# Kernel optimization log

Hardware: AMD Instinct MI355X
Metric: run time of the kernel (lower is better)

The kernel has to match this reference:

```python
import jax, jax.numpy as jnp
import numpy as np

B, S, D, H = 2, 2048, 1024, 16
HD = D // H  # 64


def setup_inputs() -> dict:
    key = jax.random.key(0)
    ks = jax.random.split(key, 7)
    s = 1.0 / np.sqrt(HD)
    return {
        "x": jax.random.normal(ks[0], (B, S, D), dtype=jnp.float32),
        "Wq": jax.random.normal(ks[1], (H, HD, HD), dtype=jnp.float32) * s,
        "bq": jax.random.normal(ks[2], (H, HD), dtype=jnp.float32) * 0.01,
        "Wk": jax.random.normal(ks[3], (H, HD, HD), dtype=jnp.float32) * s,
        "bk": jax.random.normal(ks[4], (H, HD), dtype=jnp.float32) * 0.01,
        "Wv": jax.random.normal(ks[5], (H, HD, HD), dtype=jnp.float32) * s,
        "bv": jax.random.normal(ks[6], (H, HD), dtype=jnp.float32) * 0.01,
    }


def reference(x, Wq, bq, Wk, bk, Wv, bv):
    b, s, d = x.shape
    h, hd, _ = Wq.shape
    # Faithful to torch: x.view(B, H, S, hd) is a raw reshape (mixes seq positions
    # across heads), NOT a transpose-based head split.
    xh = x.reshape(b, h, s, hd)
    # torch Linear: y @ W.T + b, with W of shape (out, in)
    q = jnp.einsum('bhse,hde->bhsd', xh, Wq) + bq[None, :, None, :]
    k = jnp.einsum('bhse,hde->bhsd', xh, Wk) + bk[None, :, None, :]
    v = jnp.einsum('bhse,hde->bhsd', xh, Wv) + bv[None, :, None, :]
    scale = 1.0 / jnp.sqrt(jnp.asarray(d / h, dtype=jnp.float32))
    attn = jax.nn.softmax(jnp.einsum('bhqd,bhkd->bhqk', q, k) * scale, axis=-1)
    out = jnp.einsum('bhqk,bhkd->bhqd', attn, v)
    # torch.cat over heads along last dim == transpose then merge
    return out.transpose(0, 2, 1, 3).reshape(b, s, d)
```

## Files before the change

### kernel.cpp

```cpp
#include <hip/hip_runtime.h>
#include <hip/hip_bf16.h>

#define BATCH 2
#define SEQ   2048
#define DMODEL 1024
#define NH    16
#define HD    64
#define QSCALE 0.1803368801111602f

typedef __attribute__((ext_vector_type(8))) short bf16x8;
typedef __attribute__((ext_vector_type(4))) float f32x4;

__device__ __forceinline__ ushort f2bf(float f) {
    union { float f; unsigned u; } v; v.f = f;
    return (ushort)((v.u + 0x8000u) >> 16);
}

__device__ __forceinline__ unsigned pack2bf(float a, float b) {
    union { float f; unsigned u; } x, y; x.f = a; y.f = b;
    return __builtin_amdgcn_perm(y.u + 0x8000u, x.u + 0x8000u, 0x07060302u);
}

__device__ __forceinline__ float exp2r(float x) {
#if __has_builtin(__builtin_amdgcn_exp2f)
    return __builtin_amdgcn_exp2f(x);
#else
    return exp2f(x);
#endif
}

#define MFMA(a, b, c) __builtin_amdgcn_mfma_f32_16x16x32_bf16((a), (b), (c), 0, 0, 0)

__global__ __launch_bounds__(256) void wfmt_kernel(
    const float* __restrict__ Wq, const float* __restrict__ Wk,
    const float* __restrict__ Wv, ushort* __restrict__ Wf)
{
    const int blk = blockIdx.x;
    const int h = blk / 3, m = blk - h * 3;
    const float* W = (m == 0 ? Wq : (m == 1 ? Wk : Wv)) + h * 4096;
    const float s = (m == 0) ? QSCALE : 1.0f;
    for (int i = 0; i < 2; ++i) {
        int idx = threadIdx.x + 256 * i;
        int l = idx & 63, chunk = idx >> 6;
        int qd = l >> 4, l16 = l & 15, nt = chunk >> 1, ks = chunk & 1;
        const float* src = W + (nt * 16 + l16) * 64 + ks * 32 + qd * 8;
        float4 a = *(const float4*)src;
        float4 b = *(const float4*)(src + 4);
        union { bf16x8 v; unsigned u[4]; } t;
        t.u[0] = pack2bf(a.x * s, a.y * s);
        t.u[1] = pack2bf(a.z * s, a.w * s);
        t.u[2] = pack2bf(b.x * s, b.y * s);
        t.u[3] = pack2bf(b.z * s, b.w * s);
        *(bf16x8*)&Wf[((size_t)blk * 512 + idx) * 8] = t.v;
    }
}

__global__ __launch_bounds__(256) void qkv_kernel(
    const float* __restrict__ x, const ushort* __restrict__ Wf,
    const float* __restrict__ bq, const float* __restrict__ bk,
    const float* __restrict__ bv,
    ushort* __restrict__ Qo, ushort* __restrict__ Kf, ushort* __restrict__ Vf)
{
    const int bid = blockIdx.x;
    const int st  = bid & 31;
    const int bh  = bid >> 5;
    const int h   = bh & (NH - 1);

    __shared__ ushort EbQ[64 * 72];
    __shared__ ushort EbK[64 * 72];
    __shared__ ushort EbV[64 * 72];

    const int tid  = threadIdx.x;
    const int wave = tid >> 6, lane = tid & 63;
    const int ln16 = lane & 15, quad = lane >> 4;

    const float* xr = x + (size_t)bh * (SEQ * HD)
                        + ((size_t)st * 64 + wave * 16 + ln16) * HD;
    bf16x8 afr[2];
#pragma unroll
    for (int ks = 0; ks < 2; ++ks) {
        const float4* p = (const float4*)(xr + ks * 32 + quad * 8);
        float4 a = p[0], b = p[1];
        union { bf16x8 v; unsigned u[4]; } t;
        t.u[0] = pack2bf(a.x, a.y);
        t.u[1] = pack2bf(a.z, a.w);
        t.u[2] = pack2bf(b.x, b.y);
        t.u[3] = pack2bf(b.z, b.w);
        afr[ks] = t.v;
    }

    const bf16x8* wf = (const bf16x8*)Wf + (size_t)h * 1536 + lane;

    f32x4 acc[3][4];
#pragma unroll
    for (int m = 0; m < 3; ++m)
#pragma unroll
        for (int nt = 0; nt < 4; ++nt) {
            f32x4 a = {0.f, 0.f, 0.f, 0.f};
            a = MFMA(afr[0], wf[(m * 8 + nt * 2 + 0) * 64], a);
            a = MFMA(afr[1], wf[(m * 8 + nt * 2 + 1) * 64], a);
            acc[m][nt] = a;
        }

#pragma unroll
    for (int nt = 0; nt < 4; ++nt) {
        float bbq = bq[h * 64 + nt * 16 + ln16] * QSCALE;
        float bbk = bk[h * 64 + nt * 16 + ln16];
#pragma unroll
        for (int r = 0; r < 4; ++r) {
            EbQ[(wave * 16 + quad * 4 + r) * 72 + nt * 16 + ln16] = f2bf(acc[0][nt][r] + bbq);
            EbK[(wave * 16 + quad * 4 + r) * 72 + nt * 16 + ln16] = f2bf(acc[1][nt][r] + bbk);
        }
        float bbv = bv[h * 64 + nt * 16 + ln16];
        ushort4 o;
        o.x = f2bf(acc[2][nt][0] + bbv);
        o.y = f2bf(acc[2][nt][1] + bbv);
        o.z = f2bf(acc[2][nt][2] + bbv);
        o.w = f2bf(acc[2][nt][3] + bbv);
        *(ushort4*)&EbV[(nt * 16 + ln16) * 72 + wave * 16 + quad * 4] = o;
    }
    __syncthreads();

    {
        ushort* dst = Qo + (size_t)bh * SEQ * HD + (size_t)st * 64 * HD;
        for (int i = 0; i < 2; ++i) {
            int idx = tid + 256 * i;
            int row = idx >> 3, c8 = (idx & 7) * 8;
            *(bf16x8*)&dst[row * 64 + c8] = *(const bf16x8*)&EbQ[row * 72 + c8];
        }
    }
    {
        ushort* dstK = Kf + ((size_t)bh * 32 + st) * 4096;
        ushort* dstV = Vf + ((size_t)bh * 32 + st) * 4096;
        for (int i = 0; i < 2; ++i) {
            int idx8 = tid + 256 * i;
            int l2 = idx8 & 63, chunk = idx8 >> 6;
            int nt = chunk >> 1, ks = chunk & 1;
            int qd = l2 >> 4, l16 = l2 & 15;
            *(bf16x8*)&dstK[(size_t)idx8 * 8] =
                *(const bf16x8*)&EbK[(nt * 16 + l16) * 72 + ks * 32 + qd * 8];
            *(bf16x8*)&dstV[(size_t)idx8 * 8] =
                *(const bf16x8*)&EbV[(nt * 16 + l16) * 72 + ks * 32 + qd * 8];
        }
    }
}

__global__ __launch_bounds__(512, 4) void attn_kernel(
    const ushort* __restrict__ Q, const ushort* __restrict__ Kf,
    const ushort* __restrict__ Vf, float* __restrict__ out)
{
    const int bid = blockIdx.x;
    const int wid = (bid & 7) * 64 + (bid >> 3);
    const int qt  = wid & 15;
    const int bh  = wid >> 4;
    const int h   = bh & (NH - 1), b = bh >> 4;

    __shared__ ushort Ps[8][2][2048];

    const int tid = threadIdx.x, wave = tid >> 6, lane = tid & 63;
    const int ln16 = lane & 15, quad = lane >> 4;
    const int qw = wave & 3, kh = wave >> 2;
    const unsigned swz = (unsigned)(ln16 & 7) << 4;

    bf16x8 qfr[2][2];
#pragma unroll
    for (int g = 0; g < 2; ++g) {
        const ushort* Qg = Q + ((size_t)bh * SEQ + qt * 128 + qw * 32 + g * 16 + ln16) * HD;
        qfr[g][0] = *(const bf16x8*)&Qg[quad * 8];
        qfr[g][1] = *(const bf16x8*)&Qg[32 + quad * 8];
    }

    const bf16x8* kfp = (const bf16x8*)(Kf + (size_t)bh * 32 * 4096) + kh * 8192 + lane;
    const bf16x8* vfp = (const bf16x8*)(Vf + (size_t)bh * 32 * 4096) + kh * 8192 + lane;

    float lsum[2] = {0.f, 0.f};
    f32x4 accO[2][4];
#pragma unroll
    for (int g = 0; g < 2; ++g)
#pragma unroll
        for (int nt = 0; nt < 4; ++nt) accO[g][nt] = (f32x4){0.f, 0.f, 0.f, 0.f};

    bf16x8 kf[8], vf[8];
#pragma unroll
    for (int c = 0; c < 8; ++c) kf[c] = kfp[c * 64];
    kfp += 512;

    for (int kt = 0; kt < 16; ++kt) {
        const int cur = kt & 1;

        f32x4 sacc[2][4];
#pragma unroll
        for (int nt = 0; nt < 4; ++nt)
#pragma unroll
            for (int g = 0; g < 2; ++g) {
                f32x4 a = {0.f, 0.f, 0.f, 0.f};
                a = MFMA(kf[nt * 2],     qfr[g][0], a);
                a = MFMA(kf[nt * 2 + 1], qfr[g][1], a);
                sacc[g][nt] = a;
            }

        if (kt < 15) {
#pragma unroll
            for (int c = 0; c < 8; ++c) kf[c] = kfp[c * 64];
            kfp += 512;
        }

        if (kt > 0) {
            const char* Pr = (const char*)Ps[wave][1 - cur];
            bf16x8 pf[2][2];
#pragma unroll
            for (int g = 0; g < 2; ++g) {
                const char* Prr = Pr + (g * 16 + ln16) * 128;
                pf[g][0] = *(const bf16x8*)(Prr + (((unsigned)(quad * 16)) ^ swz));
                pf[g][1] = *(const bf16x8*)(Prr + (((unsigned)(64 + quad * 16)) ^ swz));
            }
#pragma unroll
            for (int nt = 0; nt < 4; ++nt)
#pragma unroll
                for (int g = 0; g < 2; ++g) {
                    accO[g][nt] = MFMA(vf[nt * 2],     pf[g][0], accO[g][nt]);
                    accO[g][nt] = MFMA(vf[nt * 2 + 1], pf[g][1], accO[g][nt]);
                }
        }

#pragma unroll
        for (int c = 0; c < 8; ++c) vf[c] = vfp[c * 64];
        vfp += 512;

        char* Pw = (char*)Ps[wave][cur];
#pragma unroll
        for (int g = 0; g < 2; ++g) {
            char* Pwr = Pw + (g * 16 + ln16) * 128;
            float rs = 0.f;
#pragma unroll
            for (int nt = 0; nt < 4; ++nt) {
                float p0 = exp2r(sacc[g][nt][0]);
                float p1 = exp2r(sacc[g][nt][1]);
                float p2 = exp2r(sacc[g][nt][2]);
                float p3 = exp2r(sacc[g][nt][3]);
                rs += (p0 + p1) + (p2 + p3);
                uint2 pk;
                pk.x = pack2bf(p0, p1);
                pk.y = pack2bf(p2, p3);
                *(uint2*)(Pwr + (((unsigned)(nt * 32 + quad * 8)) ^ swz)) = pk;
            }
            lsum[g] += rs;
        }
    }

    {
        const char* Pr = (const char*)Ps[wave][1];
        bf16x8 pf[2][2];
#pragma unroll
        for (int g = 0; g < 2; ++g) {
            const char* Prr = Pr + (g * 16 + ln16) * 128;
            pf[g][0] = *(const bf16x8*)(Prr + (((unsigned)(quad * 16)) ^ swz));
            pf[g][1] = *(const bf16x8*)(Prr + (((unsigned)(64 + quad * 16)) ^ swz));
        }
#pragma unroll
        for (int nt = 0; nt < 4; ++nt)
#pragma unroll
            for (int g = 0; g < 2; ++g) {
                accO[g][nt] = MFMA(vf[nt * 2],     pf[g][0], accO[g][nt]);
                accO[g][nt] = MFMA(vf[nt * 2 + 1], pf[g][1], accO[g][nt]);
            }
    }

    __syncthreads();
    if (kh == 1) {
        float* ex = (float*)&Ps[wave][0][0];
#pragma unroll
        for (int g = 0; g < 2; ++g)
#pragma unroll
            for (int nt = 0; nt < 4; ++nt)
                *(f32x4*)&ex[((g * 4 + nt) * 64 + lane) * 4] = accO[g][nt];
        float* exl = (float*)&Ps[wave - 4][0][0];
        exl[lane * 2 + 0] = lsum[0];
        exl[lane * 2 + 1] = lsum[1];
    }
    __syncthreads();
    if (kh == 0) {
        const float* ex  = (const float*)&Ps[wave + 4][0][0];
        const float* exl = (const float*)&Ps[wave][0][0];
#pragma unroll
        for (int g = 0; g < 2; ++g)
#pragma unroll
            for (int nt = 0; nt < 4; ++nt) {
                f32x4 o = *(const f32x4*)&ex[((g * 4 + nt) * 64 + lane) * 4];
                accO[g][nt][0] += o[0]; accO[g][nt][1] += o[1];
                accO[g][nt][2] += o[2]; accO[g][nt][3] += o[3];
            }
        lsum[0] += exl[lane * 2 + 0];
        lsum[1] += exl[lane * 2 + 1];

#pragma unroll
        for (int g = 0; g < 2; ++g) {
            float l = lsum[g];
            l += __shfl_xor(l, 16, 64);
            l += __shfl_xor(l, 32, 64);
            float rinv = 1.0f / l;
            float* ob = out + ((size_t)b * SEQ + qt * 128 + qw * 32 + g * 16 + ln16) * DMODEL + h * HD;
#pragma unroll
            for (int nt = 0; nt < 4; ++nt) {
                float4 o;
                o.x = accO[g][nt][0] * rinv;
                o.y = accO[g][nt][1] * rinv;
                o.z = accO[g][nt][2] * rinv;
                o.w = accO[g][nt][3] * rinv;
                *(float4*)&ob[nt * 16 + quad * 4] = o;
            }
        }
    }
}

extern "C" void kernel_launch(void* const* d_in, const int* in_sizes, int n_in,
                              void* d_out, int out_size, void* d_ws, size_t ws_size,
                              hipStream_t stream) {
    const float* x  = (const float*)d_in[0];
    const float* Wq = (const float*)d_in[1];
    const float* bq = (const float*)d_in[2];
    const float* Wk = (const float*)d_in[3];
    const float* bk = (const float*)d_in[4];
    const float* Wv = (const float*)d_in[5];
    const float* bv = (const float*)d_in[6];

    const size_t nElem = (size_t)BATCH * NH * SEQ * HD;
    ushort* Qw  = (ushort*)d_ws;
    ushort* Kw  = Qw + nElem;
    ushort* Vw  = Kw + nElem;
    ushort* Wfw = Vw + nElem;

    wfmt_kernel<<<48, 256, 0, stream>>>(Wq, Wk, Wv, Wfw);
    qkv_kernel<<<32 * 32, 256, 0, stream>>>(
        x, Wfw, bq, bk, bv, Qw, Kw, Vw);
    attn_kernel<<<BATCH * NH * (SEQ / 128), 512, 0, stream>>>(
        Qw, Kw, Vw, (float*)d_out);
}
```

Before: 154.6 us.

## Split attention key range across separate blocks and combine partials in a new kernel

The two key halves of each query tile, previously handled by two wave groups inside one 512-thread block and merged through shared memory, now run in separate 256-thread blocks. Each block writes unnormalized partial outputs and row sums to workspace, and a new combine kernel adds the two halves and normalizes. This doubles the block count and halves per-block LDS, aiming at better occupancy and scheduling. In exchange it adds an extra kernel launch and writes then rereads two full fp32 output-sized partial buffers.

```diff
diff --git a/kernel.cpp b/kernel.cpp
--- a/kernel.cpp
+++ b/kernel.cpp
@@ -145,27 +145,28 @@
     }
 }
 
-__global__ __launch_bounds__(512, 4) void attn_kernel(
+__global__ __launch_bounds__(256, 4) void attn_part_kernel(
     const ushort* __restrict__ Q, const ushort* __restrict__ Kf,
-    const ushort* __restrict__ Vf, float* __restrict__ out)
+    const ushort* __restrict__ Vf, float* __restrict__ Opart,
+    float* __restrict__ lsumw)
 {
     const int bid = blockIdx.x;
-    const int wid = (bid & 7) * 64 + (bid >> 3);
+    const int wid = (bid & 7) * 128 + (bid >> 3);
+    const int bh  = wid >> 5;
+    const int kh  = (wid >> 4) & 1;
     const int qt  = wid & 15;
-    const int bh  = wid >> 4;
     const int h   = bh & (NH - 1), b = bh >> 4;
 
-    __shared__ ushort Ps[8][2][2048];
+    __shared__ ushort Ps[4][2][2048];
 
     const int tid = threadIdx.x, wave = tid >> 6, lane = tid & 63;
     const int ln16 = lane & 15, quad = lane >> 4;
-    const int qw = wave & 3, kh = wave >> 2;
     const unsigned swz = (unsigned)(ln16 & 7) << 4;
 
     bf16x8 qfr[2][2];
 #pragma unroll
     for (int g = 0; g < 2; ++g) {
-        const ushort* Qg = Q + ((size_t)bh * SEQ + qt * 128 + qw * 32 + g * 16 + ln16) * HD;
+        const ushort* Qg = Q + ((size_t)bh * SEQ + qt * 128 + wave * 32 + g * 16 + ln16) * HD;
         qfr[g][0] = *(const bf16x8*)&Qg[quad * 8];
         qfr[g][1] = *(const bf16x8*)&Qg[32 + quad * 8];
     }
@@ -266,50 +267,51 @@
             }
     }
 
-    __syncthreads();
-    if (kh == 1) {
-        float* ex = (float*)&Ps[wave][0][0];
-#pragma unroll
-        for (int g = 0; g < 2; ++g)
-#pragma unroll
-            for (int nt = 0; nt < 4; ++nt)
-                *(f32x4*)&ex[((g * 4 + nt) * 64 + lane) * 4] = accO[g][nt];
-        float* exl = (float*)&Ps[wave - 4][0][0];
-        exl[lane * 2 + 0] = lsum[0];
-        exl[lane * 2 + 1] = lsum[1];
-    }
-    __syncthreads();
-    if (kh == 0) {
-        const float* ex  = (const float*)&Ps[wave + 4][0][0];
-        const float* exl = (const float*)&Ps[wave][0][0];
-#pragma unroll
-        for (int g = 0; g < 2; ++g)
-#pragma unroll
-            for (int nt = 0; nt < 4; ++nt) {
-                f32x4 o = *(const f32x4*)&ex[((g * 4 + nt) * 64 + lane) * 4];
-                accO[g][nt][0] += o[0]; accO[g][nt][1] += o[1];
-                accO[g][nt][2] += o[2]; accO[g][nt][3] += o[3];
-            }
-        lsum[0] += exl[lane * 2 + 0];
-        lsum[1] += exl[lane * 2 + 1];
-
-#pragma unroll
-        for (int g = 0; g < 2; ++g) {
-            float l = lsum[g];
-            l += __shfl_xor(l, 16, 64);
-            l += __shfl_xor(l, 32, 64);
-            float rinv = 1.0f / l;
-            float* ob = out + ((size_t)b * SEQ + qt * 128 + qw * 32 + g * 16 + ln16) * DMODEL + h * HD;
-#pragma unroll
-            for (int nt = 0; nt < 4; ++nt) {
-                float4 o;
-                o.x = accO[g][nt][0] * rinv;
-                o.y = accO[g][nt][1] * rinv;
-                o.z = accO[g][nt][2] * rinv;
-                o.w = accO[g][nt][3] * rinv;
-                *(float4*)&ob[nt * 16 + quad * 4] = o;
-            }
-        }
+#pragma unroll
+    for (int g = 0; g < 2; ++g) {
+        float l = lsum[g];
+        l += __shfl_xor(l, 16, 64);
+        l += __shfl_xor(l, 32, 64);
+        const int qrow = qt * 128 + wave * 32 + g * 16 + ln16;
+        if (lane < 16)
+            lsumw[(size_t)kh * (32 * SEQ) + (size_t)bh * SEQ + qrow] = l;
+        float* ob = Opart + (size_t)kh * ((size_t)BATCH * SEQ * DMODEL)
+                  + ((size_t)b * SEQ + qrow) * DMODEL + h * HD;
+#pragma unroll
+        for (int nt = 0; nt < 4; ++nt) {
+            float4 o;
+            o.x = accO[g][nt][0];
+            o.y = accO[g][nt][1];
+            o.z = accO[g][nt][2];
+            o.w = accO[g][nt][3];
+            *(float4*)&ob[nt * 16 + quad * 4] = o;
+        }
+    }
+}
+
+__global__ __launch_bounds__(256) void combine_kernel(
+    const float* __restrict__ Opart, const float* __restrict__ lsumw,
+    float* __restrict__ out)
+{
+    const int nf4 = BATCH * SEQ * DMODEL / 4;
+    for (int i = blockIdx.x * 256 + threadIdx.x; i < nf4; i += 2048 * 256) {
+        int flat = i << 2;
+        int b = flat >> 21;
+        int rem = flat & ((1 << 21) - 1);
+        int s = rem >> 10;
+        int d = rem & (DMODEL - 1);
+        int h = d >> 6;
+        size_t li = (size_t)((b << 4) + h) * SEQ + s;
+        float l = lsumw[li] + lsumw[(size_t)32 * SEQ + li];
+        float rinv = 1.0f / l;
+        float4 o0 = ((const float4*)Opart)[i];
+        float4 o1 = ((const float4*)Opart)[i + nf4];
+        float4 o;
+        o.x = (o0.x + o1.x) * rinv;
+        o.y = (o0.y + o1.y) * rinv;
+        o.z = (o0.z + o1.z) * rinv;
+        o.w = (o0.w + o1.w) * rinv;
+        ((float4*)out)[i] = o;
     }
 }
 
@@ -325,14 +327,18 @@
     const float* bv = (const float*)d_in[6];
 
     const size_t nElem = (size_t)BATCH * NH * SEQ * HD;
-    ushort* Qw  = (ushort*)d_ws;
-    ushort* Kw  = Qw + nElem;
-    ushort* Vw  = Kw + nElem;
-    ushort* Wfw = Vw + nElem;
+    const size_t nOut  = (size_t)BATCH * SEQ * DMODEL;
+    ushort* Qw   = (ushort*)d_ws;
+    ushort* Kw   = Qw + nElem;
+    ushort* Vw   = Kw + nElem;
+    ushort* Wfw  = Vw + nElem;
+    float*  Opar = (float*)(Wfw + 48 * 512 * 8);
+    float*  lsw  = Opar + 2 * nOut;
 
     wfmt_kernel<<<48, 256, 0, stream>>>(Wq, Wk, Wv, Wfw);
     qkv_kernel<<<32 * 32, 256, 0, stream>>>(
         x, Wfw, bq, bk, bv, Qw, Kw, Vw);
-    attn_kernel<<<BATCH * NH * (SEQ / 128), 512, 0, stream>>>(
-        Qw, Kw, Vw, (float*)d_out);
-}
+    attn_part_kernel<<<32 * 2 * 16, 256, 0, stream>>>(
+        Qw, Kw, Vw, Opar, lsw);
+    combine_kernel<<<2048, 256, 0, stream>>>(Opar, lsw, (float*)d_out);
+}
```

Result: slower. 163.8 us (+5.9%).

## Split QK^T by query group and stream V fragments to cut register pressure

Applied to the files above, without the earlier changes.

Restructures the attention inner loop so scores are computed and exponentiated per 16-row query group, not both groups at once. The second group's Q fragments are reloaded from global memory each iteration instead of kept in registers. V fragments are loaded in pairs just before the PV MFMAs rather than held as an 8-register array. This lowers live vector registers, to help reach the 4-waves launch bound or avoid spills and to interleave exp work with MFMAs. The cost is repeated Q loads and less latency hiding for V loads.

```diff
diff --git a/kernel.cpp b/kernel.cpp
--- a/kernel.cpp
+++ b/kernel.cpp
@@ -162,13 +162,11 @@
     const int qw = wave & 3, kh = wave >> 2;
     const unsigned swz = (unsigned)(ln16 & 7) << 4;
 
-    bf16x8 qfr[2][2];
-#pragma unroll
-    for (int g = 0; g < 2; ++g) {
-        const ushort* Qg = Q + ((size_t)bh * SEQ + qt * 128 + qw * 32 + g * 16 + ln16) * HD;
-        qfr[g][0] = *(const bf16x8*)&Qg[quad * 8];
-        qfr[g][1] = *(const bf16x8*)&Qg[32 + quad * 8];
-    }
+    const ushort* Qg0 = Q + ((size_t)bh * SEQ + qt * 128 + qw * 32 + ln16) * HD;
+    const ushort* Qg1 = Qg0 + 16 * HD;
+    bf16x8 qfr0[2];
+    qfr0[0] = *(const bf16x8*)&Qg0[quad * 8];
+    qfr0[1] = *(const bf16x8*)&Qg0[32 + quad * 8];
 
     const bf16x8* kfp = (const bf16x8*)(Kf + (size_t)bh * 32 * 4096) + kh * 8192 + lane;
     const bf16x8* vfp = (const bf16x8*)(Vf + (size_t)bh * 32 * 4096) + kh * 8192 + lane;
@@ -180,7 +178,7 @@
 #pragma unroll
         for (int nt = 0; nt < 4; ++nt) accO[g][nt] = (f32x4){0.f, 0.f, 0.f, 0.f};
 
-    bf16x8 kf[8], vf[8];
+    bf16x8 kf[8];
 #pragma unroll
     for (int c = 0; c < 8; ++c) kf[c] = kfp[c * 64];
     kfp += 512;
@@ -188,63 +186,103 @@
     for (int kt = 0; kt < 16; ++kt) {
         const int cur = kt & 1;
 
-        f32x4 sacc[2][4];
-#pragma unroll
-        for (int nt = 0; nt < 4; ++nt)
-#pragma unroll
-            for (int g = 0; g < 2; ++g) {
-                f32x4 a = {0.f, 0.f, 0.f, 0.f};
-                a = MFMA(kf[nt * 2],     qfr[g][0], a);
-                a = MFMA(kf[nt * 2 + 1], qfr[g][1], a);
-                sacc[g][nt] = a;
-            }
-
-        if (kt < 15) {
-#pragma unroll
-            for (int c = 0; c < 8; ++c) kf[c] = kfp[c * 64];
-            kfp += 512;
-        }
-
+        f32x4 s0[4];
+#pragma unroll
+        for (int nt = 0; nt < 4; ++nt) {
+            f32x4 a = {0.f, 0.f, 0.f, 0.f};
+            a = MFMA(kf[nt * 2],     qfr0[0], a);
+            a = MFMA(kf[nt * 2 + 1], qfr0[1], a);
+            s0[nt] = a;
+        }
+
+        bf16x8 q1a = *(const bf16x8*)&Qg1[quad * 8];
+        bf16x8 q1b = *(const bf16x8*)&Qg1[32 + quad * 8];
+
+        bf16x8 vA0, vA1, vB0, vB1;
         if (kt > 0) {
-            const char* Pr = (const char*)Ps[wave][1 - cur];
-            bf16x8 pf[2][2];
-#pragma unroll
-            for (int g = 0; g < 2; ++g) {
-                const char* Prr = Pr + (g * 16 + ln16) * 128;
-                pf[g][0] = *(const bf16x8*)(Prr + (((unsigned)(quad * 16)) ^ swz));
-                pf[g][1] = *(const bf16x8*)(Prr + (((unsigned)(64 + quad * 16)) ^ swz));
-            }
-#pragma unroll
-            for (int nt = 0; nt < 4; ++nt)
-#pragma unroll
-                for (int g = 0; g < 2; ++g) {
-                    accO[g][nt] = MFMA(vf[nt * 2],     pf[g][0], accO[g][nt]);
-                    accO[g][nt] = MFMA(vf[nt * 2 + 1], pf[g][1], accO[g][nt]);
-                }
-        }
-
-#pragma unroll
-        for (int c = 0; c < 8; ++c) vf[c] = vfp[c * 64];
-        vfp += 512;
-
-        char* Pw = (char*)Ps[wave][cur];
-#pragma unroll
-        for (int g = 0; g < 2; ++g) {
-            char* Pwr = Pw + (g * 16 + ln16) * 128;
+            vA0 = vfp[0];   vA1 = vfp[64];
+            vB0 = vfp[128]; vB1 = vfp[192];
+        }
+
+        {
+            char* Pwr = (char*)Ps[wave][cur] + ln16 * 128;
             float rs = 0.f;
 #pragma unroll
             for (int nt = 0; nt < 4; ++nt) {
-                float p0 = exp2r(sacc[g][nt][0]);
-                float p1 = exp2r(sacc[g][nt][1]);
-                float p2 = exp2r(sacc[g][nt][2]);
-                float p3 = exp2r(sacc[g][nt][3]);
+                float p0 = exp2r(s0[nt][0]);
+                float p1 = exp2r(s0[nt][1]);
+                float p2 = exp2r(s0[nt][2]);
+                float p3 = exp2r(s0[nt][3]);
                 rs += (p0 + p1) + (p2 + p3);
                 uint2 pk;
                 pk.x = pack2bf(p0, p1);
                 pk.y = pack2bf(p2, p3);
                 *(uint2*)(Pwr + (((unsigned)(nt * 32 + quad * 8)) ^ swz)) = pk;
             }
-            lsum[g] += rs;
+            lsum[0] += rs;
+        }
+
+        f32x4 s1[4];
+#pragma unroll
+        for (int nt = 0; nt < 4; ++nt) {
+            f32x4 a = {0.f, 0.f, 0.f, 0.f};
+            a = MFMA(kf[nt * 2],     q1a, a);
+            a = MFMA(kf[nt * 2 + 1], q1b, a);
+            s1[nt] = a;
+        }
+
+        if (kt > 0) {
+            const char* Pr = (const char*)Ps[wave][1 - cur];
+            bf16x8 pf[2][2];
+#pragma unroll
+            for (int g = 0; g < 2; ++g) {
+                const char* Prr = Pr + (g * 16 + ln16) * 128;
+                pf[g][0] = *(const bf16x8*)(Prr + (((unsigned)(quad * 16)) ^ swz));
+                pf[g][1] = *(const bf16x8*)(Prr + (((unsigned)(64 + quad * 16)) ^ swz));
+            }
+            accO[0][0] = MFMA(vA0, pf[0][0], accO[0][0]);
+            accO[0][0] = MFMA(vA1, pf[0][1], accO[0][0]);
+            accO[1][0] = MFMA(vA0, pf[1][0], accO[1][0]);
+            accO[1][0] = MFMA(vA1, pf[1][1], accO[1][0]);
+            vA0 = vfp[256]; vA1 = vfp[320];
+            accO[0][1] = MFMA(vB0, pf[0][0], accO[0][1]);
+            accO[0][1] = MFMA(vB1, pf[0][1], accO[0][1]);
+            accO[1][1] = MFMA(vB0, pf[1][0], accO[1][1]);
+            accO[1][1] = MFMA(vB1, pf[1][1], accO[1][1]);
+            vB0 = vfp[384]; vB1 = vfp[448];
+            accO[0][2] = MFMA(vA0, pf[0][0], accO[0][2]);
+            accO[0][2] = MFMA(vA1, pf[0][1], accO[0][2]);
+            accO[1][2] = MFMA(vA0, pf[1][0], accO[1][2]);
+            accO[1][2] = MFMA(vA1, pf[1][1], accO[1][2]);
+            accO[0][3] = MFMA(vB0, pf[0][0], accO[0][3]);
+            accO[0][3] = MFMA(vB1, pf[0][1], accO[0][3]);
+            accO[1][3] = MFMA(vB0, pf[1][0], accO[1][3]);
+            accO[1][3] = MFMA(vB1, pf[1][1], accO[1][3]);
+            vfp += 512;
+        }
+
+        if (kt < 15) {
+#pragma unroll
+            for (int c = 0; c < 8; ++c) kf[c] = kfp[c * 64];
+            kfp += 512;
+        }
+
+        {
+            char* Pwr = (char*)Ps[wave][cur] + (16 + ln16) * 128;
+            float rs = 0.f;
+#pragma unroll
+            for (int nt = 0; nt < 4; ++nt) {
+                float p0 = exp2r(s1[nt][0]);
+                float p1 = exp2r(s1[nt][1]);
+                float p2 = exp2r(s1[nt][2]);
+                float p3 = exp2r(s1[nt][3]);
+                rs += (p0 + p1) + (p2 + p3);
+                uint2 pk;
+                pk.x = pack2bf(p0, p1);
+                pk.y = pack2bf(p2, p3);
+                *(uint2*)(Pwr + (((unsigned)(nt * 32 + quad * 8)) ^ swz)) = pk;
+            }
+            lsum[1] += rs;
         }
     }
 
@@ -257,13 +295,26 @@
             pf[g][0] = *(const bf16x8*)(Prr + (((unsigned)(quad * 16)) ^ swz));
             pf[g][1] = *(const bf16x8*)(Prr + (((unsigned)(64 + quad * 16)) ^ swz));
         }
-#pragma unroll
-        for (int nt = 0; nt < 4; ++nt)
-#pragma unroll
-            for (int g = 0; g < 2; ++g) {
-                accO[g][nt] = MFMA(vf[nt * 2],     pf[g][0], accO[g][nt]);
-                accO[g][nt] = MFMA(vf[nt * 2 + 1], pf[g][1], accO[g][nt]);
-            }
+        bf16x8 vA0 = vfp[0],   vA1 = vfp[64];
+        bf16x8 vB0 = vfp[128], vB1 = vfp[192];
+        accO[0][0] = MFMA(vA0, pf[0][0], accO[0][0]);
+        accO[0][0] = MFMA(vA1, pf[0][1], accO[0][0]);
+        accO[1][0] = MFMA(vA0, pf[1][0], accO[1][0]);
+        accO[1][0] = MFMA(vA1, pf[1][1], accO[1][0]);
+        vA0 = vfp[256]; vA1 = vfp[320];
+        accO[0][1] = MFMA(vB0, pf[0][0], accO[0][1]);
+        accO[0][1] = MFMA(vB1, pf[0][1], accO[0][1]);
+        accO[1][1] = MFMA(vB0, pf[1][0], accO[1][1]);
+        accO[1][1] = MFMA(vB1, pf[1][1], accO[1][1]);
+        vB0 = vfp[384]; vB1 = vfp[448];
+        accO[0][2] = MFMA(vA0, pf[0][0], accO[0][2]);
+        accO[0][2] = MFMA(vA1, pf[0][1], accO[0][2]);
+        accO[1][2] = MFMA(vA0, pf[1][0], accO[1][2]);
+        accO[1][2] = MFMA(vA1, pf[1][1], accO[1][2]);
+        accO[0][3] = MFMA(vB0, pf[0][0], accO[0][3]);
+        accO[0][3] = MFMA(vB1, pf[0][1], accO[0][3]);
+        accO[1][3] = MFMA(vB0, pf[1][0], accO[1][3]);
+        accO[1][3] = MFMA(vB1, pf[1][1], accO[1][3]);
     }
 
     __syncthreads();
```

After: 135.0 us. 12.7% less time.
